# Kernel tuning notes

Measured on AMD Instinct MI355X. Metric: run time of the kernel, lower is better.

The kernel has to match this reference:

```python
import jax, jax.numpy as jnp
import numpy as np
import math

B = 2; H = 128; W = 128
QIN = 256; INC = 256; DIM = 32; NH = 8; OUTC = 256
POINTS = 4; ATT_P = 2; OFR = 2.0; EPS = 1e-5
SCALE = DIM ** -0.5


def _make_pe():
    max_len = H * W
    pos = np.arange(max_len, dtype=np.float32)[:, None]
    div = np.exp(np.arange(0, INC, 2, dtype=np.float32) * -(math.log(10000.0) / INC))
    pe = np.zeros((max_len, INC), np.float32)
    pe[:, 0::2] = np.sin(pos * div)
    pe[:, 1::2] = np.cos(pos * div)
    return jnp.asarray(pe.T.reshape(1, INC, H, W))


PE = _make_pe()


def _ref_points():
    ry = jnp.linspace(0.5, H - 0.5, H) / (H - 1.0) * 2.0 - 1.0
    rx = jnp.linspace(0.5, W - 0.5, W) / (W - 1.0) * 2.0 - 1.0
    gy, gx = jnp.meshgrid(ry, rx, indexing='ij')
    return jnp.stack([gy, gx], -1)  # (H, W, 2) in (y, x)


REFPTS = _ref_points()


def group_norm(x, groups, gamma, beta):
    b, c, h, w = x.shape
    xr = x.reshape(b, groups, -1)
    mu = xr.mean(-1, keepdims=True)
    var = xr.var(-1, keepdims=True)
    xn = ((xr - mu) * jax.lax.rsqrt(var + EPS)).reshape(b, c, h, w)
    return xn * gamma[None, :, None, None] + beta[None, :, None, None]


def conv1x1(x, w):
    return jnp.einsum('bihw,oi->bohw', x, w)


def gconv1x1(x, w):
    # grouped 1x1 conv: x (B, G*Ci, H, W), w (G, Co, Ci) -> (B, G*Co, H, W)
    b, _, h, ww = x.shape
    g, co, ci = w.shape
    xg = x.reshape(b, g, ci, h, ww)
    return jnp.einsum('bgihw,goi->bgohw', xg, w).reshape(b, g * co, h, ww)


def grid_sample(img, grid):
    # img (N,C,H,W); grid (N,Hg,Wg,2) (x,y) in [-1,1]; bilinear, align_corners=True, zero pad
    n, c, h, w = img.shape
    gx = (grid[..., 0] + 1.0) * 0.5 * (w - 1)
    gy = (grid[..., 1] + 1.0) * 0.5 * (h - 1)
    x0 = jnp.floor(gx)
    y0 = jnp.floor(gy)
    wx1 = gx - x0; wx0 = 1.0 - wx1
    wy1 = gy - y0; wy0 = 1.0 - wy1
    flat = img.reshape(n, c, h * w)

    def tap(ix, iy, wt):
        valid = (ix >= 0) & (ix <= w - 1) & (iy >= 0) & (iy <= h - 1)
        idx = (jnp.clip(iy, 0, h - 1) * w + jnp.clip(ix, 0, w - 1)).astype(jnp.int32)
        g = jnp.take_along_axis(flat, idx.reshape(n, 1, -1), axis=2)
        return g * jnp.where(valid, wt, 0.0).reshape(n, 1, -1)

    out = (tap(x0, y0, wx0 * wy0) + tap(x0 + 1.0, y0, wx1 * wy0)
           + tap(x0, y0 + 1.0, wx0 * wy1) + tap(x0 + 1.0, y0 + 1.0, wx1 * wy1))
    return out.reshape(n, c, grid.shape[1], grid.shape[2])


def _fwd(q, x, off_w1, off_b1, off_gn_g, off_gn_b, off_w2, wq, wk, wv, wx,
         w_out, b_out, wkh, wvh, ca_w, gn1_g, gn1_b, ffn_w1, ffn_b1,
         ffn_w2, ffn_b2, gn2_g, gn2_b):
    residual1 = x
    q = q + PE
    # conv_offset: 3x3 conv -> GroupNorm(1) -> ReLU -> grouped 1x1 (no bias)
    t = jax.lax.conv_general_dilated(q, off_w1, (1, 1), ((1, 1), (1, 1)),
                                     dimension_numbers=('NCHW', 'OIHW', 'NCHW'))
    t = t + off_b1[None, :, None, None]
    t = jax.nn.relu(group_norm(t, 1, off_gn_g, off_gn_b))
    offset = gconv1x1(t, off_w2)                      # (B, NH*POINTS*2, H, W)
    offset = offset.reshape(B * NH * POINTS, 2, H, W)
    off_range = jnp.array([1.0 / (H - 1.0), 1.0 / (W - 1.0)], jnp.float32).reshape(1, 2, 1, 1)
    offset = jnp.tanh(offset) * off_range * OFR
    pos = offset.transpose(0, 2, 3, 1) + REFPTS[None]  # (B*NH*P, H, W, 2) in (y, x)

    qp = conv1x1(q, wq).reshape(B * NH, DIM, H * W)

    x = x + PE
    x = conv1x1(x, wx)                                 # (B, NH*DIM, H, W)
    # channel attention gate (adaptive max+avg pool -> shared 1x1 -> sigmoid)
    mx = x.max((2, 3))
    av = x.mean((2, 3))
    gate = jax.nn.sigmoid(mx @ ca_w.T + av @ ca_w.T)
    x_h = x + gate[:, :, None, None] * x

    kh = conv1x1(x_h, wkh).reshape(B * NH, ATT_P, DIM, H * W)
    vh = conv1x1(x_h, wvh).reshape(B * NH, ATT_P, DIM, H * W)

    # deformable sampling, vectorized over (batch, head)
    x_heads = x.reshape(B * NH, DIM, H, W)
    grid = pos.reshape(B * NH, POINTS * H, W, 2)[..., ::-1]  # (x, y)
    samp = grid_sample(x_heads, grid)                  # (B*NH, DIM, POINTS*H, W)
    samp = samp.reshape(B, NH, DIM, POINTS, H, W).transpose(0, 3, 1, 2, 4, 5)
    samp = samp.reshape(B * POINTS, NH * DIM, H, W)

    k = gconv1x1(samp, wk).reshape(B, POINTS, NH, DIM, H * W)
    k = k.transpose(0, 2, 1, 3, 4).reshape(B * NH, POINTS, DIM, H * W)
    k = jnp.concatenate([k, kh], axis=1)               # (B*NH, POINTS+2, DIM, M)
    v = gconv1x1(samp, wv).reshape(B, POINTS, NH, DIM, H * W)
    v = v.transpose(0, 2, 1, 3, 4).reshape(B * NH, POINTS, DIM, H * W)
    v = jnp.concatenate([v, vh], axis=1)

    attn = jax.nn.softmax(jnp.einsum('bcm,bpcm->bpm', qp, k) * SCALE, axis=1)
    out = jnp.einsum('bpm,bpcm->bcm', attn, v).reshape(B, NH * DIM, H, W)
    out = gconv1x1(out, w_out) + b_out[None, :, None, None]
    out = group_norm(residual1 + out, NH, gn1_g, gn1_b)
    residual2 = out
    y = jax.nn.relu(gconv1x1(out, ffn_w1) + ffn_b1[None, :, None, None])
    y = conv1x1(y, ffn_w2) + ffn_b2[None, :, None, None]
    return group_norm(y + residual2, 1, gn2_g, gn2_b)


def setup_inputs() -> dict:
    key = jax.random.key(0)
    ks = jax.random.split(key, 16)
    s = 0.05
    d = {}
    d['q'] = jax.random.normal(ks[0], (B, QIN, H, W), jnp.float32)
    d['x'] = jax.random.normal(ks[1], (B, INC, H, W), jnp.float32)
    d['off_w1'] = jax.random.normal(ks[2], (QIN, QIN, 3, 3), jnp.float32) * s
    d['off_b1'] = jnp.zeros((QIN,), jnp.float32)
    d['off_gn_g'] = jnp.ones((QIN,), jnp.float32)
    d['off_gn_b'] = jnp.zeros((QIN,), jnp.float32)
    d['off_w2'] = jax.random.normal(ks[3], (NH, 2 * POINTS, QIN // NH), jnp.float32) * s
    d['wq'] = jax.random.normal(ks[4], (NH * DIM, QIN), jnp.float32) * s
    d['wk'] = jax.random.normal(ks[5], (NH, DIM, DIM), jnp.float32) * s
    d['wv'] = jax.random.normal(ks[6], (NH, DIM, DIM), jnp.float32) * s
    d['wx'] = jax.random.normal(ks[7], (NH * DIM, INC), jnp.float32) * s
    d['w_out'] = jax.random.normal(ks[8], (NH, OUTC // NH, DIM), jnp.float32) * s
    d['b_out'] = jnp.zeros((OUTC,), jnp.float32)
    d['wkh'] = jax.random.normal(ks[9], (NH * ATT_P * DIM, INC), jnp.float32) * s
    d['wvh'] = jax.random.normal(ks[10], (NH * ATT_P * DIM, INC), jnp.float32) * s
    d['ca_w'] = jax.random.normal(ks[11], (NH * DIM, NH * DIM), jnp.float32) * s
    d['gn1_g'] = jnp.ones((OUTC,), jnp.float32)
    d['gn1_b'] = jnp.zeros((OUTC,), jnp.float32)
    d['ffn_w1'] = jax.random.normal(ks[12], (NH, 2 * OUTC // NH, OUTC // NH), jnp.float32) * s
    d['ffn_b1'] = jnp.zeros((2 * OUTC,), jnp.float32)
    d['ffn_w2'] = jax.random.normal(ks[13], (OUTC, 2 * OUTC), jnp.float32) * s
    d['ffn_b2'] = jnp.zeros((OUTC,), jnp.float32)
    d['gn2_g'] = jnp.ones((OUTC,), jnp.float32)
    d['gn2_b'] = jnp.zeros((OUTC,), jnp.float32)
    return d


def reference(q, x, off_w1, off_b1, off_gn_g, off_gn_b, off_w2, wq, wk, wv, wx,
              w_out, b_out, wkh, wvh, ca_w, gn1_g, gn1_b, ffn_w1, ffn_b1,
              ffn_w2, ffn_b2, gn2_g, gn2_b):
    return _fwd(q, x, off_w1, off_b1, off_gn_g, off_gn_b, off_w2, wq, wk, wv, wx,
                w_out, b_out, wkh, wvh, ca_w, gn1_g, gn1_b, ffn_w1, ffn_b1,
                ffn_w2, ffn_b2, gn2_g, gn2_b)
```

## Files before the change

### kernel.cpp

```cpp
#include <hip/hip_runtime.h>
#include <hip/hip_bf16.h>
#include <math.h>

typedef unsigned short u16;
typedef __attribute__((ext_vector_type(8))) unsigned short u16v8;
typedef __attribute__((ext_vector_type(8))) __bf16 bf16v8;
typedef __attribute__((ext_vector_type(4))) float f32v4;

#define BB 2
#define MM 16384
#define CC 256
#define NHH 8
#define PTS 4
#define BMTOT 32768
#define SCALEF 0.17677669529663687f
#define PECOEF 0.03597789207803197f
#define PD 131
#define PDPIX (PD*PD)

__device__ __forceinline__ u16 f2bf(float f) {
    union { float f; unsigned u; } v; v.f = f;
    unsigned u = v.u;
    return (u16)((u + 0x7fffu + ((u >> 16) & 1u)) >> 16);
}
__device__ __forceinline__ float bf2f(u16 u) {
    union { unsigned u; float f; } v; v.u = ((unsigned)u) << 16; return v.f;
}
__device__ __forceinline__ float rsum32(float v) {
    #pragma unroll
    for (int m = 16; m; m >>= 1) v += __shfl_xor(v, m, 32);
    return v;
}
__device__ __forceinline__ void gload16(const void* g, void* l) {
    __builtin_amdgcn_global_load_lds(
        (const __attribute__((address_space(1))) void*)g,
        (__attribute__((address_space(3))) void*)l, 16, 0, 0);
}

__global__ __launch_bounds__(256)
void prep_kernel(const float* __restrict__ off_w1, const float* __restrict__ wq,
                 const float* __restrict__ wx, const float* __restrict__ fw2,
                 u16* zp, u16* w1t, u16* wqb, u16* wxb, u16* fw2b)
{
    const size_t n_zp = 128, n_w1 = 589824, n_q = 65536, n_f2 = 131072;
    const size_t total = n_zp + n_w1 + 2 * n_q + n_f2;
    for (size_t i = (size_t)blockIdx.x * 256 + threadIdx.x; i < total;
         i += (size_t)gridDim.x * 256) {
        size_t j = i;
        if (j < n_zp) { zp[j] = 0; continue; }
        j -= n_zp;
        if (j < n_w1) {
            size_t oc = j / 2304, r = j % 2304, tap = r >> 8, ic = r & 255;
            w1t[j] = f2bf(off_w1[(oc * 256 + ic) * 9 + tap]);
            continue;
        }
        j -= n_w1;
        if (j < n_q) { wqb[j] = f2bf(wq[j] * SCALEF); continue; }
        j -= n_q;
        if (j < n_q) { wxb[j] = f2bf(wx[j]); continue; }
        j -= n_q;
        fw2b[j] = f2bf(fw2[j]);
    }
}

__global__ __launch_bounds__(256)
void addpe_kernel(const float* __restrict__ q, const float* __restrict__ x,
                  u16* __restrict__ qpe, u16* __restrict__ xpe)
{
    __shared__ float lq[64][65], lx[64][65];
    const int m0 = blockIdx.x * 64, c0 = blockIdx.y * 64, b = blockIdx.z;
    const int tid = threadIdx.x;
    {
        const int ml = tid & 63, c4 = tid >> 6;
        for (int s = 0; s < 16; ++s) {
            int cl = s * 4 + c4;
            int c = c0 + cl, m = m0 + ml;
            float dv = __expf(-(float)(c & ~1) * PECOEF);
            float a = (float)m * dv;
            float pe = (c & 1) ? __cosf(a) : __sinf(a);
            size_t gi = ((size_t)b * CC + c) * MM + m;
            lq[cl][ml] = q[gi] + pe;
            lx[cl][ml] = x[gi] + pe;
        }
    }
    __syncthreads();
    {
        const int cl = tid & 63, m4 = tid >> 6;
        for (int s = 0; s < 16; ++s) {
            int ml = s * 4 + m4;
            size_t oi = ((size_t)b * MM + m0 + ml) * CC + c0 + cl;
            qpe[oi] = f2bf(lq[cl][ml]);
            xpe[oi] = f2bf(lx[cl][ml]);
        }
    }
}

template<int AMODE, int OUTBF>
__global__ __launch_bounds__(256, 2)
void gemm_bt(const u16* __restrict__ A, const u16* __restrict__ Bw,
             const float* __restrict__ bias, void* __restrict__ Cout,
             int K, int N, const u16* __restrict__ zp)
{
    __shared__ u16 lA[128 * 32];
    __shared__ u16 lB[128 * 32];
    const int tid = threadIdx.x;
    const int w = tid >> 6, l = tid & 63;
    const int gm = blockIdx.x, gn = blockIdx.y;
    const int wm = w >> 1, wn = w & 1;
    const int rowIn = l >> 2;
    const int kc = (l & 3) << 3;
    f32v4 acc[4][4] = {};

    for (int k0 = 0; k0 < K; k0 += 32) {
        #pragma unroll
        for (int r = 0; r < 2; ++r) {
            const int seg = r * 4 + w;
            const int row = seg * 16 + rowIn;
            const u16* gpA;
            if (AMODE == 0) {
                gpA = A + (size_t)(gm * 128 + row) * K + (k0 + kc);
            } else {
                int grow = gm * 128 + row;
                int bimg = grow >> 14, m = grow & 16383;
                int y = m >> 7, xx2 = m & 127;
                int kk2 = k0 + kc;
                int tap = kk2 >> 8, ic = kk2 & 255;
                int t3 = tap / 3;
                int py = y + t3 - 1, px = xx2 + (tap - t3 * 3) - 1;
                bool ok = ((unsigned)py < 128u) && ((unsigned)px < 128u);
                gpA = ok ? (A + (((size_t)((bimg << 14) + (py << 7) + px)) << 8) + ic) : zp;
            }
            gload16(gpA, lA + seg * 512);
            const u16* gpB = Bw + (size_t)(gn * 128 + row) * K + (k0 + kc);
            gload16(gpB, lB + seg * 512);
        }
        __syncthreads();
        bf16v8 af[4], bf[4];
        #pragma unroll
        for (int i = 0; i < 4; ++i) {
            af[i] = *(const bf16v8*)&lA[((wm << 6) + (i << 4) + (l & 15)) * 32 + ((l >> 4) << 3)];
            bf[i] = *(const bf16v8*)&lB[((wn << 6) + (i << 4) + (l & 15)) * 32 + ((l >> 4) << 3)];
        }
        #pragma unroll
        for (int i = 0; i < 4; ++i)
            #pragma unroll
            for (int j = 0; j < 4; ++j)
                acc[i][j] = __builtin_amdgcn_mfma_f32_16x16x32_bf16(af[i], bf[j], acc[i][j], 0, 0, 0);
        __syncthreads();
    }

    const int l15 = l & 15, l4 = l >> 4;
    #pragma unroll
    for (int i = 0; i < 4; ++i) {
        int row = gm * 128 + (wm << 6) + (i << 4) + (l4 << 2);
        #pragma unroll
        for (int j = 0; j < 4; ++j) {
            int col = gn * 128 + (wn << 6) + (j << 4) + l15;
            float bv = bias ? bias[col] : 0.0f;
            #pragma unroll
            for (int r = 0; r < 4; ++r) {
                float val = acc[i][j][r] + bv;
                if (OUTBF) ((u16*)Cout)[(size_t)(row + r) * N + col] = f2bf(val);
                else       ((float*)Cout)[(size_t)(row + r) * N + col] = val;
            }
        }
    }
}

__global__ __launch_bounds__(256)
void stats1_bf_kernel(const u16* __restrict__ a, float* __restrict__ part)
{
    __shared__ float ls[256], lss[256];
    const int blk = blockIdx.x;
    const int bb = blk >> 5, ch = blk & 31;
    const size_t base = ((size_t)bb * MM + ch * 512) * CC;
    const int tid = threadIdx.x;
    float s = 0.f, ss = 0.f;
    for (int p = 0; p < 512; ++p) {
        float v = bf2f(a[base + (size_t)p * CC + tid]);
        s += v; ss += v * v;
    }
    ls[tid] = s; lss[tid] = ss;
    __syncthreads();
    if (tid < 8) {
        float S = 0.f, SS = 0.f;
        for (int j = 0; j < 32; ++j) { S += ls[tid * 32 + j]; SS += lss[tid * 32 + j]; }
        part[(blk * 8 + tid) * 2] = S;
        part[(blk * 8 + tid) * 2 + 1] = SS;
    }
}

__global__ __launch_bounds__(256)
void stats1_mix_kernel(const float* __restrict__ a, const u16* __restrict__ r1raw,
                       const float2* __restrict__ st1, const float* __restrict__ g1g,
                       const float* __restrict__ g1b, float* __restrict__ part)
{
    __shared__ float ls[256], lss[256];
    const int blk = blockIdx.x;
    const int bb = blk >> 5, ch = blk & 31;
    const size_t base = ((size_t)bb * MM + ch * 512) * CC;
    const int tid = threadIdx.x;
    const float2 st = st1[bb * 8 + (tid >> 5)];
    const float gg = g1g[tid], gb = g1b[tid];
    float s = 0.f, ss = 0.f;
    for (int p = 0; p < 512; ++p) {
        float rv = (bf2f(r1raw[base + (size_t)p * CC + tid]) - st.x) * st.y * gg + gb;
        float v = a[base + (size_t)p * CC + tid] + rv;
        s += v; ss += v * v;
    }
    ls[tid] = s; lss[tid] = ss;
    __syncthreads();
    if (tid < 8) {
        float S = 0.f, SS = 0.f;
        for (int j = 0; j < 32; ++j) { S += ls[tid * 32 + j]; SS += lss[tid * 32 + j]; }
        part[(blk * 8 + tid) * 2] = S;
        part[(blk * 8 + tid) * 2 + 1] = SS;
    }
}

__global__ __launch_bounds__(64)
void stats2_kernel(const float* __restrict__ part, float2* __restrict__ stats, int NG)
{
    const int t = threadIdx.x;
    if (t >= 2 * NG) return;
    const int bb = t / NG, g = t % NG;
    const int gsub = 8 / NG;
    float S = 0.f, SS = 0.f;
    for (int ch = 0; ch < 32; ++ch)
        for (int j = 0; j < gsub; ++j) {
            int idx = (bb * 32 + ch) * 8 + g * gsub + j;
            S += part[idx * 2]; SS += part[idx * 2 + 1];
        }
    const float cnt = (256.0f / NG) * 16384.0f;
    float mu = S / cnt;
    float var = SS / cnt - mu * mu;
    stats[bb * NG + g] = make_float2(mu, rsqrtf(var + 1e-5f));
}

__global__ __launch_bounds__(256)
void offset_kernel(const u16* __restrict__ t, const float2* __restrict__ stats_t,
                   const float* __restrict__ gng, const float* __restrict__ gnb,
                   const float* __restrict__ w2, u16* __restrict__ pos)
{
    __shared__ float lt[4 * 256];
    const int tid = threadIdx.x;
    const int bm0 = blockIdx.x * 4;
    const int b = bm0 >> 14;
    const float2 st = stats_t[b];
    for (int idx = tid; idx < 1024; idx += 256) {
        int pix = idx >> 8, c = idx & 255;
        float v = bf2f(t[(size_t)(bm0 + pix) * CC + c]);
        v = (v - st.x) * st.y * gng[c] + gnb[c];
        lt[idx] = fmaxf(v, 0.0f);
    }
    __syncthreads();
    const int pix = tid >> 6, go = tid & 63;
    const int g = go >> 3, o = go & 7;
    float s = 0.f;
    #pragma unroll
    for (int ci = 0; ci < 32; ++ci) {
        int ce = (ci + g * 4) & 31;
        s += w2[(g * 8 + o) * 32 + ce] * lt[pix * 256 + g * 32 + ce];
    }
    const int m = (bm0 + pix) & 16383;
    const int p = o >> 1, c2 = o & 1;
    pos[((((size_t)b * NHH + g) * PTS + p) * MM + m) * 2 + c2] = f2bf(tanhf(s));
}

__global__ __launch_bounds__(256)
void pool1_kernel(const u16* __restrict__ xc, float* __restrict__ pmax,
                  float* __restrict__ psum)
{
    const int blk = blockIdx.x;
    const int bb = blk >> 5, ch = blk & 31;
    const size_t base = ((size_t)bb * MM + ch * 512) * CC;
    const int tid = threadIdx.x;
    float mx = -1e30f, s = 0.f;
    for (int p = 0; p < 512; ++p) {
        float v = bf2f(xc[base + (size_t)p * CC + tid]);
        mx = fmaxf(mx, v); s += v;
    }
    pmax[blk * 256 + tid] = mx;
    psum[blk * 256 + tid] = s;
}

__global__ __launch_bounds__(256)
void pool2_gate_kernel(const float* __restrict__ pmax, const float* __restrict__ psum,
                       const float* __restrict__ ca_w, float* __restrict__ gate)
{
    __shared__ float sv[256];
    const int bb = blockIdx.x, tid = threadIdx.x;
    float mx = -1e30f, s = 0.f;
    for (int ch = 0; ch < 32; ++ch) {
        mx = fmaxf(mx, pmax[(bb * 32 + ch) * 256 + tid]);
        s += psum[(bb * 32 + ch) * 256 + tid];
    }
    sv[tid] = mx + s * (1.0f / 16384.0f);
    __syncthreads();
    float acc = 0.f;
    for (int ci = 0; ci < 256; ++ci) acc += ca_w[tid * 256 + ci] * sv[ci];
    gate[bb * 256 + tid] = 1.0f / (1.0f + __expf(-acc));
}

__global__ __launch_bounds__(256)
void scalekv_kernel(const float* __restrict__ wkh, const float* __restrict__ wvh,
                    const float* __restrict__ gate, u16* __restrict__ wkhs,
                    u16* __restrict__ wvhs)
{
    const int n1 = 512 * 256;
    for (int i = blockIdx.x * 256 + threadIdx.x; i < 4 * n1;
         i += gridDim.x * 256) {
        int which = i / (2 * n1);
        int r = i % (2 * n1);
        int b = r / n1, j = r % n1;
        float gsc = 1.0f + gate[b * 256 + (j & 255)];
        if (which == 0) wkhs[b * n1 + j] = f2bf(wkh[j] * gsc);
        else            wvhs[b * n1 + j] = f2bf(wvh[j] * gsc);
    }
}

__global__ __launch_bounds__(256)
void padzero_kernel(u16* __restrict__ xckv)
{
    const int total = 2 * 777 * 256;
    for (int i = blockIdx.x * 256 + threadIdx.x; i < total;
         i += gridDim.x * 256) {
        int b = i / (777 * 256);
        int r = i % (777 * 256);
        int pix = r >> 8, w = r & 255;
        int py, px;
        if (pix < 393) {
            int rr = pix / PD;
            py = (rr == 0) ? 0 : (128 + rr);
            px = pix - rr * PD;
        } else {
            int r2 = pix - 393;
            py = 1 + r2 / 3;
            int cc = r2 % 3;
            px = (cc == 0) ? 0 : (128 + cc);
        }
        *(unsigned*)&xckv[(((size_t)b * PDPIX + py * PD + px) << 9) + w * 2] = 0u;
    }
}

__global__ __launch_bounds__(256)
void projkv_kernel(const u16* __restrict__ xc, const float* __restrict__ wk,
                   const float* __restrict__ wv, u16* __restrict__ xckv)
{
    __shared__ float la[256];
    const int tid = threadIdx.x;
    const int g = tid >> 5;
    float wkr[32], wvr[32];
    #pragma unroll
    for (int dd = 0; dd < 32; ++dd) {
        wkr[dd] = wk[tid * 32 + dd];
        wvr[dd] = wv[tid * 32 + dd];
    }
    const int m0 = blockIdx.x * 32;
    for (int i = 0; i < 32; ++i) {
        const size_t bm = m0 + i;
        la[tid] = bf2f(xc[bm * CC + tid]);
        __syncthreads();
        float ok = 0.f, ov = 0.f;
        #pragma unroll
        for (int dd = 0; dd < 32; ++dd) {
            ok += wkr[dd] * la[g * 32 + dd];
            ov += wvr[dd] * la[g * 32 + dd];
        }
        unsigned pack = (unsigned)f2bf(ok) | ((unsigned)f2bf(ov) << 16);
        const int b = (int)(bm >> 14), m = (int)(bm & 16383);
        const int y = m >> 7, x = m & 127;
        *(unsigned*)&xckv[(((size_t)b * PDPIX + (y + 1) * PD + (x + 1)) << 9) + tid * 2] = pack;
        __syncthreads();
    }
}

__global__ __launch_bounds__(256)
void attn_kernel(const u16* __restrict__ qp, const u16* __restrict__ xckv,
                 const u16* __restrict__ kh, const u16* __restrict__ vh,
                 const u16* __restrict__ pos, u16* __restrict__ attno)
{
    const int tid = threadIdx.x;
    const int g = tid >> 5, d = tid & 31;
    const int bh = blockIdx.y;
    const int b = bh >> 3, nh = bh & 7;
    const int co = nh * 32 + d;
    const size_t hb = (size_t)b * MM;
    const u16* xb = xckv + (((size_t)b * PDPIX) << 9) + co * 2;
    #pragma unroll
    for (int i = 0; i < 4; ++i) {
        const int m = blockIdx.x * 32 + i * 8 + g;
        const size_t bm = hb + m;
        const float qd = bf2f(qp[bm * CC + co]);
        const int yy = m >> 7, xx = m & 127;
        float kk[6], vv[6];
        #pragma unroll
        for (int p = 0; p < 4; ++p) {
            unsigned pxy = *(const unsigned*)&pos[((((size_t)b * NHH + nh) * PTS + p) * MM + m) * 2];
            float gy = (float)yy + 0.5f + bf2f((u16)pxy);
            float gx = (float)xx + 0.5f + bf2f((u16)(pxy >> 16));
            float fy0 = floorf(gy), fx0 = floorf(gx);
            int iy0 = (int)fy0, ix0 = (int)fx0;
            float fx = gx - fx0, fy = gy - fy0;
            float w00 = (1.f - fx) * (1.f - fy), w10 = fx * (1.f - fy);
            float w01 = (1.f - fx) * fy, w11 = fx * fy;
            const u16* t0 = xb + ((size_t)((iy0 + 1) * PD + ix0 + 1) << 9);
            unsigned kv00 = *(const unsigned*)t0;
            unsigned kv10 = *(const unsigned*)(t0 + 512);
            unsigned kv01 = *(const unsigned*)(t0 + PD * 512);
            unsigned kv11 = *(const unsigned*)(t0 + PD * 512 + 512);
            kk[p] = w00 * bf2f((u16)kv00) + w10 * bf2f((u16)kv10)
                  + w01 * bf2f((u16)kv01) + w11 * bf2f((u16)kv11);
            vv[p] = w00 * bf2f((u16)(kv00 >> 16)) + w10 * bf2f((u16)(kv10 >> 16))
                  + w01 * bf2f((u16)(kv01 >> 16)) + w11 * bf2f((u16)(kv11 >> 16));
        }
        #pragma unroll
        for (int p = 0; p < 2; ++p) {
            kk[4 + p] = bf2f(kh[bm * 512 + nh * 64 + p * 32 + d]);
            vv[4 + p] = bf2f(vh[bm * 512 + nh * 64 + p * 32 + d]);
        }
        float s[6];
        #pragma unroll
        for (int p = 0; p < 6; ++p) s[p] = rsum32(qd * kk[p]);
        float mx = s[0];
        #pragma unroll
        for (int p = 1; p < 6; ++p) mx = fmaxf(mx, s[p]);
        float es[6], ssum = 0.f;
        #pragma unroll
        for (int p = 0; p < 6; ++p) { es[p] = __expf(s[p] - mx); ssum += es[p]; }
        const float inv = 1.0f / ssum;
        float od = 0.f;
        #pragma unroll
        for (int p = 0; p < 6; ++p) od += es[p] * inv * vv[p];
        attno[bm * CC + co] = f2bf(od);
    }
}

__global__ __launch_bounds__(256)
void r1_kernel(const u16* __restrict__ attno, const float* __restrict__ w_out,
               const float* __restrict__ b_out, const float* __restrict__ x_in,
               u16* __restrict__ r1)
{
    __shared__ float la[256];
    const int tid = threadIdx.x;
    const int g = tid >> 5;
    float wr[32];
    #pragma unroll
    for (int dd = 0; dd < 32; ++dd) wr[dd] = w_out[tid * 32 + dd];
    const float bo = b_out[tid];
    const int m0 = blockIdx.x * 32;
    for (int i = 0; i < 32; ++i) {
        const size_t bm = m0 + i;
        la[tid] = bf2f(attno[bm * CC + tid]);
        __syncthreads();
        float o = 0.f;
        #pragma unroll
        for (int dd = 0; dd < 32; ++dd) o += wr[dd] * la[g * 32 + dd];
        const int b = (int)(bm >> 14), m = (int)(bm & 16383);
        float xv = x_in[((size_t)b * CC + tid) * MM + m];
        r1[bm * CC + tid] = f2bf(xv + o + bo);
        __syncthreads();
    }
}

__global__ __launch_bounds__(256)
void ffn1_kernel(const u16* __restrict__ r1raw, const float2* __restrict__ st1,
                 const float* __restrict__ g1g, const float* __restrict__ g1b,
                 const float* __restrict__ w1, const float* __restrict__ b1,
                 u16* __restrict__ y1bf)
{
    __shared__ float la[256];
    const int tid = threadIdx.x;
    float wr0[32], wr1[32];
    #pragma unroll
    for (int dd = 0; dd < 32; ++dd) {
        wr0[dd] = w1[tid * 32 + dd];
        wr1[dd] = w1[(tid + 256) * 32 + dd];
    }
    const float bb0 = b1[tid], bb1 = b1[tid + 256];
    const int g0 = tid >> 6, g1 = 4 + (tid >> 6);
    const int m0 = blockIdx.x * 32;
    const int bb = m0 >> 14;
    const float2 st = st1[bb * 8 + (tid >> 5)];
    const float gg = g1g[tid], gb = g1b[tid];
    for (int i = 0; i < 32; ++i) {
        const size_t bm = m0 + i;
        la[tid] = (bf2f(r1raw[bm * CC + tid]) - st.x) * st.y * gg + gb;
        __syncthreads();
        float o0 = bb0, o1 = bb1;
        #pragma unroll
        for (int dd = 0; dd < 32; ++dd) {
            o0 += wr0[dd] * la[g0 * 32 + dd];
            o1 += wr1[dd] * la[g1 * 32 + dd];
        }
        y1bf[bm * 512 + tid] = f2bf(fmaxf(o0, 0.f));
        y1bf[bm * 512 + tid + 256] = f2bf(fmaxf(o1, 0.f));
        __syncthreads();
    }
}

__global__ __launch_bounds__(256)
void final_kernel(const float* __restrict__ y2, const u16* __restrict__ r1raw,
                  const float2* __restrict__ st1, const float* __restrict__ g1g,
                  const float* __restrict__ g1b, const float2* __restrict__ stats,
                  const float* __restrict__ gg, const float* __restrict__ gb,
                  float* __restrict__ out)
{
    __shared__ float lt[64][65];
    const int m0 = blockIdx.x * 64, c0 = blockIdx.y * 64, b = blockIdx.z;
    const int tid = threadIdx.x;
    const float2 st = stats[b];
    {
        const int cl = tid & 63, m4 = tid >> 6;
        const int c = c0 + cl;
        const float2 s1 = st1[b * 8 + (c >> 5)];
        const float g1 = g1g[c], b1 = g1b[c];
        for (int s = 0; s < 16; ++s) {
            int ml = s * 4 + m4;
            size_t idx = ((size_t)b * MM + m0 + ml) * CC + c;
            float rv = (bf2f(r1raw[idx]) - s1.x) * s1.y * g1 + b1;
            float v = y2[idx] + rv;
            lt[cl][ml] = (v - st.x) * st.y * gg[c] + gb[c];
        }
    }
    __syncthreads();
    {
        const int mlw = tid & 63, c4 = tid >> 6;
        for (int s = 0; s < 16; ++s) {
            int clw = s * 4 + c4;
            out[((size_t)b * CC + c0 + clw) * MM + m0 + mlw] = lt[clw][mlw];
        }
    }
}

__global__ void sentinel_kernel(float* out) { out[threadIdx.x] = 1000.0f; }

extern "C" void kernel_launch(void* const* d_in, const int* in_sizes, int n_in,
                              void* d_out, int out_size, void* d_ws, size_t ws_size,
                              hipStream_t stream)
{
    const float* q_in   = (const float*)d_in[0];
    const float* x_in   = (const float*)d_in[1];
    const float* off_w1 = (const float*)d_in[2];
    const float* off_b1 = (const float*)d_in[3];
    const float* off_gn_g = (const float*)d_in[4];
    const float* off_gn_b = (const float*)d_in[5];
    const float* off_w2 = (const float*)d_in[6];
    const float* wq     = (const float*)d_in[7];
    const float* wk     = (const float*)d_in[8];
    const float* wv     = (const float*)d_in[9];
    const float* wx     = (const float*)d_in[10];
    const float* w_out  = (const float*)d_in[11];
    const float* b_out  = (const float*)d_in[12];
    const float* wkh    = (const float*)d_in[13];
    const float* wvh    = (const float*)d_in[14];
    const float* ca_w   = (const float*)d_in[15];
    const float* gn1_g  = (const float*)d_in[16];
    const float* gn1_b  = (const float*)d_in[17];
    const float* ffn_w1 = (const float*)d_in[18];
    const float* ffn_b1 = (const float*)d_in[19];
    const float* ffn_w2 = (const float*)d_in[20];
    const float* ffn_b2 = (const float*)d_in[21];
    const float* gn2_g  = (const float*)d_in[22];
    const float* gn2_b  = (const float*)d_in[23];
    float* out = (float*)d_out;

    char* W = (char*)d_ws;
    size_t off = 0;
    auto AL = [&](size_t sz) -> char* {
        char* p = W + off;
        off += (sz + 255) & ~(size_t)255;
        return p;
    };
    u16* zp    = (u16*)AL(256);
    u16* w1t   = (u16*)AL(589824 * 2);
    u16* wqb   = (u16*)AL(65536 * 2);
    u16* wxb   = (u16*)AL(65536 * 2);
    u16* fw2b  = (u16*)AL(131072 * 2);
    u16* wkhs  = (u16*)AL(2 * 131072 * 2);
    u16* wvhs  = (u16*)AL(2 * 131072 * 2);
    u16* slotA = (u16*)AL((size_t)BMTOT * CC * 2);
    u16* slotC = (u16*)AL((size_t)BMTOT * CC * 2);
    u16* slotD = (u16*)AL((size_t)BMTOT * CC * 2);
    u16* slotB = (u16*)AL((size_t)BMTOT * CC * 2);
    u16* slotE = (u16*)AL((size_t)BMTOT * CC * 2 + 1591296);
    u16* slotG = (u16*)AL((size_t)BMTOT * 512 * 2);
    u16* pos   = (u16*)AL((size_t)BB * NHH * PTS * MM * 2 * 2);
    float* part  = (float*)AL(64 * 8 * 2 * 4);
    float* pmax  = (float*)AL(64 * 256 * 4);
    float* psum  = (float*)AL(64 * 256 * 4);
    float* gate  = (float*)AL(2 * 256 * 4);
    float2* stats_t  = (float2*)AL(2 * sizeof(float2));
    float2* stats_g1 = (float2*)AL(16 * sizeof(float2));
    float2* stats_g2 = (float2*)AL(2 * sizeof(float2));

    u16* qpe = slotA;  u16* attno = slotA;
    u16* t_b = slotC;  u16* xc  = slotC;
    u16* qp  = slotD;
    u16* xpe = slotB;
    u16* xckv = slotB;
    u16* r1  = slotB;
    u16* vh  = slotG;  u16* y1bf = slotG;
    u16* kh  = (u16*)d_out;
    float* y2 = (float*)slotA;

    if (off > ws_size) {
        sentinel_kernel<<<1, 256, 0, stream>>>(out);
        return;
    }

    prep_kernel<<<3329, 256, 0, stream>>>(off_w1, wq, wx, ffn_w2,
                                          zp, w1t, wqb, wxb, fw2b);
    addpe_kernel<<<dim3(256, 4, 2), 256, 0, stream>>>(q_in, x_in, qpe, xpe);

    gemm_bt<1, 1><<<dim3(256, 2), 256, 0, stream>>>(qpe, w1t, off_b1, t_b, 2304, 256, zp);
    stats1_bf_kernel<<<64, 256, 0, stream>>>(t_b, part);
    stats2_kernel<<<1, 64, 0, stream>>>(part, stats_t, 1);
    offset_kernel<<<8192, 256, 0, stream>>>(t_b, stats_t, off_gn_g, off_gn_b, off_w2, pos);

    gemm_bt<0, 1><<<dim3(256, 2), 256, 0, stream>>>(qpe, wqb, nullptr, qp, 256, 256, zp);
    gemm_bt<0, 1><<<dim3(256, 2), 256, 0, stream>>>(xpe, wxb, nullptr, xc, 256, 256, zp);
    pool1_kernel<<<64, 256, 0, stream>>>(xc, pmax, psum);
    pool2_gate_kernel<<<2, 256, 0, stream>>>(pmax, psum, ca_w, gate);
    scalekv_kernel<<<2048, 256, 0, stream>>>(wkh, wvh, gate, wkhs, wvhs);
    padzero_kernel<<<1555, 256, 0, stream>>>(xckv);
    projkv_kernel<<<1024, 256, 0, stream>>>(xc, wk, wv, xckv);

    for (int b = 0; b < 2; ++b) {
        gemm_bt<0, 1><<<dim3(128, 4), 256, 0, stream>>>(
            xc + (size_t)b * MM * CC, wkhs + (size_t)b * 131072, nullptr,
            kh + (size_t)b * MM * 512, 256, 512, zp);
        gemm_bt<0, 1><<<dim3(128, 4), 256, 0, stream>>>(
            xc + (size_t)b * MM * CC, wvhs + (size_t)b * 131072, nullptr,
            vh + (size_t)b * MM * 512, 256, 512, zp);
    }

    attn_kernel<<<dim3(512, 16), 256, 0, stream>>>(qp, xckv, kh, vh, pos, attno);

    r1_kernel<<<1024, 256, 0, stream>>>(attno, w_out, b_out, x_in, r1);
    stats1_bf_kernel<<<64, 256, 0, stream>>>(r1, part);
    stats2_kernel<<<1, 64, 0, stream>>>(part, stats_g1, 8);

    ffn1_kernel<<<1024, 256, 0, stream>>>(r1, stats_g1, gn1_g, gn1_b,
                                          ffn_w1, ffn_b1, y1bf);
    gemm_bt<0, 0><<<dim3(256, 2), 256, 0, stream>>>(y1bf, fw2b, ffn_b2, y2, 512, 256, zp);

    stats1_mix_kernel<<<64, 256, 0, stream>>>(y2, r1, stats_g1, gn1_g, gn1_b, part);
    stats2_kernel<<<1, 64, 0, stream>>>(part, stats_g2, 1);
    final_kernel<<<dim3(256, 4, 2), 256, 0, stream>>>(y2, r1, stats_g1, gn1_g, gn1_b,
                                                      stats_g2, gn2_g, gn2_b, out);
}
```

Baseline: 724.5 us.

## Widen reduction grids and stage r1/ffn1 inputs in shared memory

The stats, pooling and mixed-stats reduction kernels now launch 512 blocks of 64 pixels instead of 64 blocks of 512, so many more CUs share these memory-bound passes. The second-stage reductions are parallelised across 256 threads with a shared-memory tree to absorb the larger partial arrays. r1_kernel and ffn1_kernel now load a whole 32-pixel tile into LDS once, coalescing the transposed x_in reads and removing two barriers per pixel. The tiles are stored as bf16, and ffn1 applies the group norm before that rounding, which adds an extra rounding step.

```diff
diff --git a/kernel.cpp b/kernel.cpp
--- a/kernel.cpp
+++ b/kernel.cpp
@@ -172,11 +172,10 @@
 {
     __shared__ float ls[256], lss[256];
     const int blk = blockIdx.x;
-    const int bb = blk >> 5, ch = blk & 31;
-    const size_t base = ((size_t)bb * MM + ch * 512) * CC;
+    const size_t base = (size_t)blk * 64 * CC;
     const int tid = threadIdx.x;
     float s = 0.f, ss = 0.f;
-    for (int p = 0; p < 512; ++p) {
+    for (int p = 0; p < 64; ++p) {
         float v = bf2f(a[base + (size_t)p * CC + tid]);
         s += v; ss += v * v;
     }
@@ -197,15 +196,16 @@
 {
     __shared__ float ls[256], lss[256];
     const int blk = blockIdx.x;
-    const int bb = blk >> 5, ch = blk & 31;
-    const size_t base = ((size_t)bb * MM + ch * 512) * CC;
+    const int bb = blk >> 8;
+    const size_t base = (size_t)blk * 64 * CC;
     const int tid = threadIdx.x;
     const float2 st = st1[bb * 8 + (tid >> 5)];
-    const float gg = g1g[tid], gb = g1b[tid];
+    const float gg = g1g[tid] * st.y;
+    const float gb = g1b[tid] - st.x * st.y * g1g[tid];
     float s = 0.f, ss = 0.f;
-    for (int p = 0; p < 512; ++p) {
-        float rv = (bf2f(r1raw[base + (size_t)p * CC + tid]) - st.x) * st.y * gg + gb;
-        float v = a[base + (size_t)p * CC + tid] + rv;
+    for (int p = 0; p < 64; ++p) {
+        float v = a[base + (size_t)p * CC + tid]
+                + bf2f(r1raw[base + (size_t)p * CC + tid]) * gg + gb;
         s += v; ss += v * v;
     }
     ls[tid] = s; lss[tid] = ss;
@@ -218,23 +218,31 @@
     }
 }
 
-__global__ __launch_bounds__(64)
+__global__ __launch_bounds__(256)
 void stats2_kernel(const float* __restrict__ part, float2* __restrict__ stats, int NG)
 {
+    __shared__ float ls[256], lss[256];
+    const int P = 2 * NG, TP = 256 / P;
     const int t = threadIdx.x;
-    if (t >= 2 * NG) return;
-    const int bb = t / NG, g = t % NG;
-    const int gsub = 8 / NG;
+    const int pr = t / TP, sub = t % TP;
+    const int bb = pr / NG, g = pr % NG;
+    const int j0 = (NG == 8) ? g : 0, jn = (NG == 8) ? 1 : 8;
     float S = 0.f, SS = 0.f;
-    for (int ch = 0; ch < 32; ++ch)
-        for (int j = 0; j < gsub; ++j) {
-            int idx = (bb * 32 + ch) * 8 + g * gsub + j;
-            S += part[idx * 2]; SS += part[idx * 2 + 1];
-        }
-    const float cnt = (256.0f / NG) * 16384.0f;
-    float mu = S / cnt;
-    float var = SS / cnt - mu * mu;
-    stats[bb * NG + g] = make_float2(mu, rsqrtf(var + 1e-5f));
+    for (int q = sub; q < 256; q += TP)
+        for (int j = 0; j < jn; ++j) {
+            int idx = ((bb * 256 + q) * 8 + j0 + j) * 2;
+            S += part[idx]; SS += part[idx + 1];
+        }
+    ls[t] = S; lss[t] = SS;
+    __syncthreads();
+    if (sub == 0) {
+        float S2 = 0.f, SS2 = 0.f;
+        for (int k = 0; k < TP; ++k) { S2 += ls[pr * TP + k]; SS2 += lss[pr * TP + k]; }
+        const float cnt = (256.0f / NG) * 16384.0f;
+        float mu = S2 / cnt;
+        float var = SS2 / cnt - mu * mu;
+        stats[bb * NG + g] = make_float2(mu, rsqrtf(var + 1e-5f));
+    }
 }
 
 __global__ __launch_bounds__(256)
@@ -272,11 +280,10 @@
                   float* __restrict__ psum)
 {
     const int blk = blockIdx.x;
-    const int bb = blk >> 5, ch = blk & 31;
-    const size_t base = ((size_t)bb * MM + ch * 512) * CC;
+    const size_t base = (size_t)blk * 64 * CC;
     const int tid = threadIdx.x;
     float mx = -1e30f, s = 0.f;
-    for (int p = 0; p < 512; ++p) {
+    for (int p = 0; p < 64; ++p) {
         float v = bf2f(xc[base + (size_t)p * CC + tid]);
         mx = fmaxf(mx, v); s += v;
     }
@@ -291,9 +298,9 @@
     __shared__ float sv[256];
     const int bb = blockIdx.x, tid = threadIdx.x;
     float mx = -1e30f, s = 0.f;
-    for (int ch = 0; ch < 32; ++ch) {
-        mx = fmaxf(mx, pmax[(bb * 32 + ch) * 256 + tid]);
-        s += psum[(bb * 32 + ch) * 256 + tid];
+    for (int q = 0; q < 256; ++q) {
+        mx = fmaxf(mx, pmax[(bb * 256 + q) * 256 + tid]);
+        s += psum[(bb * 256 + q) * 256 + tid];
     }
     sv[tid] = mx + s * (1.0f / 16384.0f);
     __syncthreads();
@@ -441,25 +448,38 @@
                const float* __restrict__ b_out, const float* __restrict__ x_in,
                u16* __restrict__ r1)
 {
-    __shared__ float la[256];
-    const int tid = threadIdx.x;
+    __shared__ u16 lx[256][36];
+    __shared__ u16 lat[32][256];
+    const int tid = threadIdx.x;
+    const int m0 = blockIdx.x * 32;
+    const int b = m0 >> 14;
+    const int mloc = m0 & 16383;
+    {
+        const int ml4 = (tid & 7) * 4, c32 = tid >> 3;
+        for (int s = 0; s < 8; ++s) {
+            int cl = s * 32 + c32;
+            float4 v = *(const float4*)&x_in[((size_t)b * CC + cl) * MM + mloc + ml4];
+            ushort4 sv = { f2bf(v.x), f2bf(v.y), f2bf(v.z), f2bf(v.w) };
+            *(ushort4*)&lx[cl][ml4] = sv;
+        }
+    }
+    {
+        const uint4* src4 = (const uint4*)(attno + (size_t)m0 * CC);
+        uint4* dst4 = (uint4*)&lat[0][0];
+        #pragma unroll
+        for (int s = 0; s < 4; ++s) dst4[s * 256 + tid] = src4[s * 256 + tid];
+    }
+    __syncthreads();
     const int g = tid >> 5;
     float wr[32];
     #pragma unroll
     for (int dd = 0; dd < 32; ++dd) wr[dd] = w_out[tid * 32 + dd];
     const float bo = b_out[tid];
-    const int m0 = blockIdx.x * 32;
     for (int i = 0; i < 32; ++i) {
-        const size_t bm = m0 + i;
-        la[tid] = bf2f(attno[bm * CC + tid]);
-        __syncthreads();
-        float o = 0.f;
-        #pragma unroll
-        for (int dd = 0; dd < 32; ++dd) o += wr[dd] * la[g * 32 + dd];
-        const int b = (int)(bm >> 14), m = (int)(bm & 16383);
-        float xv = x_in[((size_t)b * CC + tid) * MM + m];
-        r1[bm * CC + tid] = f2bf(xv + o + bo);
-        __syncthreads();
+        float o = bo + bf2f(lx[tid][i]);
+        #pragma unroll
+        for (int dd = 0; dd < 32; ++dd) o += wr[dd] * bf2f(lat[i][g * 32 + dd]);
+        r1[(size_t)(m0 + i) * CC + tid] = f2bf(o);
     }
 }
 
@@ -469,8 +489,37 @@
                  const float* __restrict__ w1, const float* __restrict__ b1,
                  u16* __restrict__ y1bf)
 {
-    __shared__ float la[256];
-    const int tid = threadIdx.x;
+    __shared__ u16 ln[32][256];
+    const int tid = threadIdx.x;
+    const int m0 = blockIdx.x * 32;
+    const int b = m0 >> 14;
+    {
+        const uint4* src4 = (const uint4*)(r1raw + (size_t)m0 * CC);
+        uint4* dst4 = (uint4*)&ln[0][0];
+        const int cbase = (tid & 31) * 8;
+        const float2 st = st1[b * 8 + (cbase >> 5)];
+        float ga[8], bb2[8];
+        #pragma unroll
+        for (int k = 0; k < 8; ++k) {
+            ga[k] = g1g[cbase + k] * st.y;
+            bb2[k] = g1b[cbase + k] - st.x * st.y * g1g[cbase + k];
+        }
+        #pragma unroll
+        for (int s = 0; s < 4; ++s) {
+            uint4 v = src4[s * 256 + tid];
+            unsigned wv[4] = { v.x, v.y, v.z, v.w };
+            unsigned ow[4];
+            #pragma unroll
+            for (int q = 0; q < 4; ++q) {
+                float lo = bf2f((u16)wv[q]) * ga[2 * q] + bb2[2 * q];
+                float hi = bf2f((u16)(wv[q] >> 16)) * ga[2 * q + 1] + bb2[2 * q + 1];
+                ow[q] = (unsigned)f2bf(lo) | ((unsigned)f2bf(hi) << 16);
+            }
+            uint4 o4; o4.x = ow[0]; o4.y = ow[1]; o4.z = ow[2]; o4.w = ow[3];
+            dst4[s * 256 + tid] = o4;
+        }
+    }
+    __syncthreads();
     float wr0[32], wr1[32];
     #pragma unroll
     for (int dd = 0; dd < 32; ++dd) {
@@ -479,23 +528,15 @@
     }
     const float bb0 = b1[tid], bb1 = b1[tid + 256];
     const int g0 = tid >> 6, g1 = 4 + (tid >> 6);
-    const int m0 = blockIdx.x * 32;
-    const int bb = m0 >> 14;
-    const float2 st = st1[bb * 8 + (tid >> 5)];
-    const float gg = g1g[tid], gb = g1b[tid];
     for (int i = 0; i < 32; ++i) {
-        const size_t bm = m0 + i;
-        la[tid] = (bf2f(r1raw[bm * CC + tid]) - st.x) * st.y * gg + gb;
-        __syncthreads();
         float o0 = bb0, o1 = bb1;
         #pragma unroll
         for (int dd = 0; dd < 32; ++dd) {
-            o0 += wr0[dd] * la[g0 * 32 + dd];
-            o1 += wr1[dd] * la[g1 * 32 + dd];
-        }
-        y1bf[bm * 512 + tid] = f2bf(fmaxf(o0, 0.f));
-        y1bf[bm * 512 + tid + 256] = f2bf(fmaxf(o1, 0.f));
-        __syncthreads();
+            o0 += wr0[dd] * bf2f(ln[i][g0 * 32 + dd]);
+            o1 += wr1[dd] * bf2f(ln[i][g1 * 32 + dd]);
+        }
+        y1bf[(size_t)(m0 + i) * 512 + tid] = f2bf(fmaxf(o0, 0.f));
+        y1bf[(size_t)(m0 + i) * 512 + tid + 256] = f2bf(fmaxf(o1, 0.f));
     }
 }
 
@@ -586,9 +627,9 @@
     u16* slotE = (u16*)AL((size_t)BMTOT * CC * 2 + 1591296);
     u16* slotG = (u16*)AL((size_t)BMTOT * 512 * 2);
     u16* pos   = (u16*)AL((size_t)BB * NHH * PTS * MM * 2 * 2);
-    float* part  = (float*)AL(64 * 8 * 2 * 4);
-    float* pmax  = (float*)AL(64 * 256 * 4);
-    float* psum  = (float*)AL(64 * 256 * 4);
+    float* part  = (float*)AL(512 * 8 * 2 * 4);
+    float* pmax  = (float*)AL(512 * 256 * 4);
+    float* psum  = (float*)AL(512 * 256 * 4);
     float* gate  = (float*)AL(2 * 256 * 4);
     float2* stats_t  = (float2*)AL(2 * sizeof(float2));
     float2* stats_g1 = (float2*)AL(16 * sizeof(float2));
@@ -614,13 +655,13 @@
     addpe_kernel<<<dim3(256, 4, 2), 256, 0, stream>>>(q_in, x_in, qpe, xpe);
 
     gemm_bt<1, 1><<<dim3(256, 2), 256, 0, stream>>>(qpe, w1t, off_b1, t_b, 2304, 256, zp);
-    stats1_bf_kernel<<<64, 256, 0, stream>>>(t_b, part);
-    stats2_kernel<<<1, 64, 0, stream>>>(part, stats_t, 1);
+    stats1_bf_kernel<<<512, 256, 0, stream>>>(t_b, part);
+    stats2_kernel<<<1, 256, 0, stream>>>(part, stats_t, 1);
     offset_kernel<<<8192, 256, 0, stream>>>(t_b, stats_t, off_gn_g, off_gn_b, off_w2, pos);
 
     gemm_bt<0, 1><<<dim3(256, 2), 256, 0, stream>>>(qpe, wqb, nullptr, qp, 256, 256, zp);
     gemm_bt<0, 1><<<dim3(256, 2), 256, 0, stream>>>(xpe, wxb, nullptr, xc, 256, 256, zp);
-    pool1_kernel<<<64, 256, 0, stream>>>(xc, pmax, psum);
+    pool1_kernel<<<512, 256, 0, stream>>>(xc, pmax, psum);
     pool2_gate_kernel<<<2, 256, 0, stream>>>(pmax, psum, ca_w, gate);
     scalekv_kernel<<<2048, 256, 0, stream>>>(wkh, wvh, gate, wkhs, wvhs);
     padzero_kernel<<<1555, 256, 0, stream>>>(xckv);
@@ -638,15 +679,15 @@
     attn_kernel<<<dim3(512, 16), 256, 0, stream>>>(qp, xckv, kh, vh, pos, attno);
 
     r1_kernel<<<1024, 256, 0, stream>>>(attno, w_out, b_out, x_in, r1);
-    stats1_bf_kernel<<<64, 256, 0, stream>>>(r1, part);
-    stats2_kernel<<<1, 64, 0, stream>>>(part, stats_g1, 8);
+    stats1_bf_kernel<<<512, 256, 0, stream>>>(r1, part);
+    stats2_kernel<<<1, 256, 0, stream>>>(part, stats_g1, 8);
 
     ffn1_kernel<<<1024, 256, 0, stream>>>(r1, stats_g1, gn1_g, gn1_b,
                                           ffn_w1, ffn_b1, y1bf);
     gemm_bt<0, 0><<<dim3(256, 2), 256, 0, stream>>>(y1bf, fw2b, ffn_b2, y2, 512, 256, zp);
 
-    stats1_mix_kernel<<<64, 256, 0, stream>>>(y2, r1, stats_g1, gn1_g, gn1_b, part);
-    stats2_kernel<<<1, 64, 0, stream>>>(part, stats_g2, 1);
+    stats1_mix_kernel<<<512, 256, 0, stream>>>(y2, r1, stats_g1, gn1_g, gn1_b, part);
+    stats2_kernel<<<1, 256, 0, stream>>>(part, stats_g2, 1);
     final_kernel<<<dim3(256, 4, 2), 256, 0, stream>>>(y2, r1, stats_g1, gn1_g, gn1_b,
                                                       stats_g2, gn2_g, gn2_b, out);
 }
```

After: 596.4 us. 1.21x faster.
